# Performance work log

Hardware: AMD Instinct MI355X
Metric: run time of the kernel (lower is better)

The kernel has to match this reference:

```python
import jax, jax.numpy as jnp
import numpy as np

N_NODES = 50000
N_EDGES = 800000
N_GRAPHS = 512
HIDDEN = 256
NODE_FEAT = 9
LAYERS = 4


def setup_inputs() -> dict:
    key = jax.random.key(0)
    ks = jax.random.split(key, 9)
    x = jax.random.normal(ks[0], (N_NODES, NODE_FEAT), dtype=jnp.float32)
    edge_index = jax.random.randint(ks[1], (2, N_EDGES), 0, N_NODES, dtype=jnp.int64)
    batch = jnp.sort(jax.random.randint(ks[2], (N_NODES,), 0, N_GRAPHS, dtype=jnp.int64))
    embed_W = jax.random.normal(ks[3], (NODE_FEAT, HIDDEN), dtype=jnp.float32) * (1.0 / np.sqrt(NODE_FEAT))
    embed_b = jnp.zeros((HIDDEN,), dtype=jnp.float32)
    conv_W = jax.random.normal(ks[4], (LAYERS, HIDDEN, HIDDEN), dtype=jnp.float32) * (1.0 / np.sqrt(HIDDEN))
    conv_b = jnp.zeros((LAYERS, HIDDEN), dtype=jnp.float32)
    out_W = jax.random.normal(ks[5], (HIDDEN, 1), dtype=jnp.float32) * (1.0 / np.sqrt(HIDDEN))
    out_b = jnp.zeros((1,), dtype=jnp.float32)
    return {"x": x, "edge_index": edge_index, "batch": batch,
            "embed_W": embed_W, "embed_b": embed_b,
            "conv_W": conv_W, "conv_b": conv_b,
            "out_W": out_W, "out_b": out_b}


def reference(x, edge_index, batch, embed_W, embed_b, conv_W, conv_b, out_W, out_b):
    n = x.shape[0]
    src, dst = edge_index[0], edge_index[1]
    # GCN symmetric normalization with self-loops: deg includes the self-loop (+1)
    deg = jax.ops.segment_sum(jnp.ones(src.shape[0], x.dtype), dst, num_segments=n) + 1.0
    dinv = jax.lax.rsqrt(deg)                       # [N]
    norm_e = dinv[src] * dinv[dst]                  # [E] edge coefficient
    self_coef = (dinv * dinv)[:, None]              # [N,1] self-loop coefficient

    h = jax.nn.relu(x @ embed_W + embed_b)          # [N,H]
    for l in range(conv_W.shape[0]):
        hw = h @ conv_W[l]                          # [N,H] transform first
        msg = hw[src] * norm_e[:, None]             # [E,H] gather + scale
        agg = jax.ops.segment_sum(msg, dst, num_segments=n)  # scatter-add
        agg = agg + hw * self_coef                  # self-loop contribution
        h = jax.nn.relu(agg + conv_b[l])

    # global mean pool over graph ids
    sums = jax.ops.segment_sum(h, batch, num_segments=N_GRAPHS)           # [G,H]
    cnt = jax.ops.segment_sum(jnp.ones(n, h.dtype), batch, num_segments=N_GRAPHS)
    pooled = sums / jnp.maximum(cnt, 1.0)[:, None]
    return pooled @ out_W + out_b                   # [G,1]
```

## Files before the change

kernel.cpp:

```cpp
#include <hip/hip_runtime.h>

#define N_NODES 50000
#define N_EDGES 800000
#define N_GRAPHS 512
#define HIDDEN 256
#define NODE_FEAT 9
#define LAYERS 4
#define BUCKET 64

typedef float floatx4 __attribute__((ext_vector_type(4)));
typedef short short8 __attribute__((ext_vector_type(8)));

__device__ __forceinline__ float bf2f(unsigned u) {
    unsigned v = u << 16;
    float f;
    __builtin_memcpy(&f, &v, 4);
    return f;
}
__device__ __forceinline__ unsigned short f2bf(float f) {
    unsigned v;
    __builtin_memcpy(&v, &f, 4);
    v += 0x7FFFu + ((v >> 16) & 1u);
    return (unsigned short)(v >> 16);
}

__global__ void fillb_kernel(const int* __restrict__ src, const int* __restrict__ dst,
                             int* __restrict__ cnt, int* __restrict__ col_src, int E) {
    int e = blockIdx.x * blockDim.x + threadIdx.x;
    if (e < E) {
        int d = dst[e];
        int pos = atomicAdd(&cnt[d], 1);
        if (pos < BUCKET) col_src[d * BUCKET + pos] = src[e];
    }
}

__global__ void dinv_kernel(const int* __restrict__ cnt, float* __restrict__ dinv, int N) {
    int i = blockIdx.x * blockDim.x + threadIdx.x;
    if (i < N) dinv[i] = rsqrtf((float)(cnt[i] + 1));
}

__global__ void findstart_kernel(const int* __restrict__ batch, int* __restrict__ gstart) {
    int g = blockIdx.x * blockDim.x + threadIdx.x;
    if (g > N_GRAPHS) return;
    if (g == N_GRAPHS) { gstart[g] = N_NODES; return; }
    int lo = 0, hi = N_NODES;
    while (lo < hi) {
        int mid = (lo + hi) >> 1;
        if (batch[mid] < g) lo = mid + 1; else hi = mid;
    }
    gstart[g] = lo;
}

__global__ __launch_bounds__(256) void packW_kernel(const float* __restrict__ W,
                                                    unsigned short* __restrict__ Wsw) {
    int idx = blockIdx.x * 256 + threadIdx.x;
    int lane = idx & 63;
    int ct   = (idx >> 6) & 15;
    int ks   = (idx >> 10) & 7;
    int l    = idx >> 13;
    int n = ct * 16 + (lane & 15);
    int kbase = ks * 32 + (lane >> 4) * 8;
    const float* Wl = W + (size_t)l * HIDDEN * HIDDEN;
    alignas(16) unsigned short tmp[8];
    #pragma unroll
    for (int j = 0; j < 8; j++)
        tmp[j] = f2bf(Wl[(size_t)(kbase + j) * HIDDEN + n]);
    *(uint4*)&Wsw[(size_t)idx * 8] = *(const uint4*)tmp;
}

__global__ __launch_bounds__(256) void embed_kernel(const float* __restrict__ x,
                                                    const float* __restrict__ W,
                                                    const float* __restrict__ b,
                                                    unsigned short* __restrict__ h) {
    int n = blockIdx.x;
    int c = threadIdx.x;
    float acc = b[c];
    #pragma unroll
    for (int k = 0; k < NODE_FEAT; k++)
        acc += x[n * NODE_FEAT + k] * W[k * HIDDEN + c];
    h[(size_t)n * HIDDEN + c] = f2bf(fmaxf(acc, 0.0f));
}

__global__ __launch_bounds__(256, 2) void gemm_mfma(const unsigned short* __restrict__ hin,
                                                    const unsigned short* __restrict__ Wsw,
                                                    unsigned short* __restrict__ hwout, int N) {
    __shared__ unsigned short As[64][264];
    int t = threadIdx.x;
    int wv = t >> 6, lane = t & 63, quad = lane >> 4, l15 = lane & 15;
    int n0 = blockIdx.x * 64;
    const uint4* h4 = (const uint4*)hin;

    uint4 av[8];
    #pragma unroll
    for (int i = 0; i < 8; i++) {
        int j = t + i * 256;
        int r = j >> 5;
        int c = j & 31;
        int n = n0 + r;
        av[i] = make_uint4(0u, 0u, 0u, 0u);
        if (n < N) av[i] = h4[(size_t)n * 32 + c];
    }
    const short8* Wl = (const short8*)Wsw;
    short8 bq[3][4];
    #pragma unroll
    for (int p = 0; p < 2; p++)
        #pragma unroll
        for (int ci = 0; ci < 4; ci++)
            bq[p][ci] = Wl[(size_t)(p * 16 + wv * 4 + ci) * 64 + lane];
    #pragma unroll
    for (int i = 0; i < 8; i++) {
        int j = t + i * 256;
        int r = j >> 5;
        int c = j & 31;
        *(uint4*)&As[r][c * 8] = av[i];
    }
    __syncthreads();

    floatx4 acc[4][4];
    #pragma unroll
    for (int i = 0; i < 4; i++)
        #pragma unroll
        for (int j = 0; j < 4; j++)
            acc[i][j] = (floatx4){0.f, 0.f, 0.f, 0.f};

    #pragma unroll
    for (int ks = 0; ks < 8; ks++) {
        if (ks < 6) {
            #pragma unroll
            for (int ci = 0; ci < 4; ci++)
                bq[(ks + 2) % 3][ci] = Wl[(size_t)((ks + 2) * 16 + wv * 4 + ci) * 64 + lane];
        }
        short8 a[4];
        #pragma unroll
        for (int rt = 0; rt < 4; rt++)
            a[rt] = *(const short8*)&As[rt * 16 + l15][ks * 32 + quad * 8];
        #pragma unroll
        for (int rt = 0; rt < 4; rt++)
            #pragma unroll
            for (int ci = 0; ci < 4; ci++)
                acc[rt][ci] = __builtin_amdgcn_mfma_f32_16x16x32_bf16(a[rt], bq[ks % 3][ci], acc[rt][ci], 0, 0, 0);
    }

    __syncthreads();
    #pragma unroll
    for (int rt = 0; rt < 4; rt++) {
        #pragma unroll
        for (int ci = 0; ci < 4; ci++) {
            int col = (wv * 4 + ci) * 16 + l15;
            int rowb = rt * 16 + quad * 4;
            #pragma unroll
            for (int reg = 0; reg < 4; reg++)
                As[rowb + reg][col] = f2bf(acc[rt][ci][reg]);
        }
    }
    __syncthreads();
    #pragma unroll
    for (int i = 0; i < 8; i++) {
        int j = t + i * 256;
        int r = j >> 5;
        int c = j & 31;
        int n = n0 + r;
        if (n < N)
            *(uint4*)&hwout[(size_t)n * HIDDEN + c * 8] = *(const uint4*)&As[r][c * 8];
    }
}

__global__ __launch_bounds__(256) void agg_kernel(const unsigned short* __restrict__ hw,
                                                  const int* __restrict__ cnt,
                                                  const int* __restrict__ col_src,
                                                  const float* __restrict__ dinv,
                                                  const float* __restrict__ bias,
                                                  unsigned short* __restrict__ hout) {
    __shared__ uint2 sEdge[4][64];
    int wv = threadIdx.x >> 6, lane = threadIdx.x & 63;
    int n = blockIdx.x * 4 + wv;
    if (n >= N_NODES) return;
    float dn = dinv[n];
    int deg = cnt[n]; if (deg > BUCKET) deg = BUCKET;

    uint2 s2 = ((const uint2*)(hw + (size_t)n * HIDDEN))[lane];
    float4 b4 = *(const float4*)&bias[4 * lane];
    float selfc = dn * dn;
    float a0 = bf2f(s2.x & 0xFFFFu) * selfc + b4.x;
    float a1 = bf2f(s2.x >> 16)     * selfc + b4.y;
    float a2 = bf2f(s2.y & 0xFFFFu) * selfc + b4.z;
    float a3 = bf2f(s2.y >> 16)     * selfc + b4.w;

    if (lane < deg) {
        int s = col_src[n * BUCKET + lane];
        float nr = dinv[s] * dn;
        unsigned nrb;
        __builtin_memcpy(&nrb, &nr, 4);
        sEdge[wv][lane] = make_uint2((unsigned)s, nrb);
    }
    for (int i = 0; i < deg; i++) {
        uint2 p = sEdge[wv][i];
        float nr;
        __builtin_memcpy(&nr, &p.y, 4);
        uint2 u = ((const uint2*)(hw + (size_t)p.x * HIDDEN))[lane];
        a0 += nr * bf2f(u.x & 0xFFFFu);
        a1 += nr * bf2f(u.x >> 16);
        a2 += nr * bf2f(u.y & 0xFFFFu);
        a3 += nr * bf2f(u.y >> 16);
    }
    unsigned p0 = (unsigned)f2bf(fmaxf(a0, 0.0f)) | ((unsigned)f2bf(fmaxf(a1, 0.0f)) << 16);
    unsigned p1 = (unsigned)f2bf(fmaxf(a2, 0.0f)) | ((unsigned)f2bf(fmaxf(a3, 0.0f)) << 16);
    ((uint2*)(hout + (size_t)n * HIDDEN))[lane] = make_uint2(p0, p1);
}

__global__ __launch_bounds__(256) void pool2_kernel(const unsigned short* __restrict__ h,
                                                    const int* __restrict__ gstart,
                                                    const float* __restrict__ outW,
                                                    const float* __restrict__ outb,
                                                    float* __restrict__ out) {
    __shared__ float sred[4];
    int g = blockIdx.x;
    int t = threadIdx.x;
    int s = gstart[g], e = gstart[g + 1];
    int half = t >> 7;
    int tc = t & 127;
    float w0 = outW[2 * tc], w1 = outW[2 * tc + 1];
    float acc = 0.0f;
    for (int n = s + half; n < e; n += 2) {
        unsigned u = *(const unsigned*)&h[(size_t)n * HIDDEN + 2 * tc];
        acc += w0 * bf2f(u & 0xFFFFu) + w1 * bf2f(u >> 16);
    }
    #pragma unroll
    for (int off = 32; off > 0; off >>= 1) acc += __shfl_down(acc, off, 64);
    if ((t & 63) == 0) sred[t >> 6] = acc;
    __syncthreads();
    if (t == 0) {
        float tot = sred[0] + sred[1] + sred[2] + sred[3];
        float cntf = (float)(e - s);
        out[g] = tot / fmaxf(cntf, 1.0f) + outb[0];
    }
}

extern "C" void kernel_launch(void* const* d_in, const int* in_sizes, int n_in,
                              void* d_out, int out_size, void* d_ws, size_t ws_size,
                              hipStream_t stream) {
    const float* x     = (const float*)d_in[0];
    const int*   edge  = (const int*)d_in[1];
    const int*   src   = edge;
    const int*   dst   = edge + N_EDGES;
    const int*   batch = (const int*)d_in[2];
    const float* embW  = (const float*)d_in[3];
    const float* embb  = (const float*)d_in[4];
    const float* convW = (const float*)d_in[5];
    const float* convb = (const float*)d_in[6];
    const float* outW  = (const float*)d_in[7];
    const float* outb  = (const float*)d_in[8];
    float* out = (float*)d_out;

    char* ws = (char*)d_ws;
    size_t off = 0;
    auto take = [&](size_t bytes) { char* p = ws + off; off += (bytes + 255) & ~(size_t)255; return p; };
    int*   cnt     = (int*)  take((size_t)N_NODES * 4);
    int*   col_src = (int*)  take((size_t)N_NODES * BUCKET * 4);
    float* dinv    = (float*)take((size_t)N_NODES * 4);
    int*   gstart  = (int*)  take((size_t)(N_GRAPHS + 1) * 4);
    unsigned short* Wsw = (unsigned short*)take((size_t)LAYERS * 8 * 16 * 64 * 8 * 2);
    unsigned short* h0  = (unsigned short*)take((size_t)N_NODES * HIDDEN * 2);
    unsigned short* h1  = (unsigned short*)take((size_t)N_NODES * HIDDEN * 2);

    hipMemsetAsync(cnt, 0, (size_t)N_NODES * 4, stream);

    fillb_kernel<<<(N_EDGES + 255) / 256, 256, 0, stream>>>(src, dst, cnt, col_src, N_EDGES);
    dinv_kernel<<<(N_NODES + 255) / 256, 256, 0, stream>>>(cnt, dinv, N_NODES);
    findstart_kernel<<<3, 256, 0, stream>>>(batch, gstart);

    packW_kernel<<<128, 256, 0, stream>>>(convW, Wsw);
    embed_kernel<<<N_NODES, 256, 0, stream>>>(x, embW, embb, h0);

    unsigned short* ha = h0;
    unsigned short* hb = h1;
    for (int l = 0; l < LAYERS; l++) {
        gemm_mfma<<<(N_NODES + 63) / 64, 256, 0, stream>>>(ha, Wsw + (size_t)l * 65536, hb, N_NODES);
        agg_kernel<<<(N_NODES + 3) / 4, 256, 0, stream>>>(hb, cnt, col_src, dinv, convb + (size_t)l * HIDDEN, ha);
    }

    pool2_kernel<<<N_GRAPHS, 256, 0, stream>>>(ha, gstart, outW, outb, out);
}
```

Baseline: 459.7 us.

## Split each wavefront across two nodes with 16-byte gathers and unrolled edge loop

```diff
diff --git a/kernel.cpp b/kernel.cpp
--- a/kernel.cpp
+++ b/kernel.cpp
@@ -165,47 +165,87 @@
     }
 }
 
+__device__ __forceinline__ void acc8(float* a, uint4 u, float nr) {
+    a[0] += nr * bf2f(u.x & 0xFFFFu); a[1] += nr * bf2f(u.x >> 16);
+    a[2] += nr * bf2f(u.y & 0xFFFFu); a[3] += nr * bf2f(u.y >> 16);
+    a[4] += nr * bf2f(u.z & 0xFFFFu); a[5] += nr * bf2f(u.z >> 16);
+    a[6] += nr * bf2f(u.w & 0xFFFFu); a[7] += nr * bf2f(u.w >> 16);
+}
+
 __global__ __launch_bounds__(256) void agg_kernel(const unsigned short* __restrict__ hw,
                                                   const int* __restrict__ cnt,
                                                   const int* __restrict__ col_src,
                                                   const float* __restrict__ dinv,
                                                   const float* __restrict__ bias,
                                                   unsigned short* __restrict__ hout) {
-    __shared__ uint2 sEdge[4][64];
+    __shared__ uint2 sEdge[4][2][BUCKET];
     int wv = threadIdx.x >> 6, lane = threadIdx.x & 63;
-    int n = blockIdx.x * 4 + wv;
+    int half = lane >> 5, q = lane & 31;
+    int n = blockIdx.x * 8 + wv * 2 + half;
     if (n >= N_NODES) return;
     float dn = dinv[n];
     int deg = cnt[n]; if (deg > BUCKET) deg = BUCKET;
 
-    uint2 s2 = ((const uint2*)(hw + (size_t)n * HIDDEN))[lane];
-    float4 b4 = *(const float4*)&bias[4 * lane];
+    if (q < deg) {
+        int s = col_src[n * BUCKET + q];
+        float nr = dinv[s] * dn;
+        unsigned nrb; __builtin_memcpy(&nrb, &nr, 4);
+        sEdge[wv][half][q] = make_uint2((unsigned)s, nrb);
+    }
+    if (q + 32 < deg) {
+        int s = col_src[n * BUCKET + q + 32];
+        float nr = dinv[s] * dn;
+        unsigned nrb; __builtin_memcpy(&nrb, &nr, 4);
+        sEdge[wv][half][q + 32] = make_uint2((unsigned)s, nrb);
+    }
+
+    uint4 s4 = ((const uint4*)(hw + (size_t)n * HIDDEN))[q];
     float selfc = dn * dn;
-    float a0 = bf2f(s2.x & 0xFFFFu) * selfc + b4.x;
-    float a1 = bf2f(s2.x >> 16)     * selfc + b4.y;
-    float a2 = bf2f(s2.y & 0xFFFFu) * selfc + b4.z;
-    float a3 = bf2f(s2.y >> 16)     * selfc + b4.w;
-
-    if (lane < deg) {
-        int s = col_src[n * BUCKET + lane];
-        float nr = dinv[s] * dn;
-        unsigned nrb;
-        __builtin_memcpy(&nrb, &nr, 4);
-        sEdge[wv][lane] = make_uint2((unsigned)s, nrb);
-    }
-    for (int i = 0; i < deg; i++) {
-        uint2 p = sEdge[wv][i];
-        float nr;
-        __builtin_memcpy(&nr, &p.y, 4);
-        uint2 u = ((const uint2*)(hw + (size_t)p.x * HIDDEN))[lane];
-        a0 += nr * bf2f(u.x & 0xFFFFu);
-        a1 += nr * bf2f(u.x >> 16);
-        a2 += nr * bf2f(u.y & 0xFFFFu);
-        a3 += nr * bf2f(u.y >> 16);
-    }
-    unsigned p0 = (unsigned)f2bf(fmaxf(a0, 0.0f)) | ((unsigned)f2bf(fmaxf(a1, 0.0f)) << 16);
-    unsigned p1 = (unsigned)f2bf(fmaxf(a2, 0.0f)) | ((unsigned)f2bf(fmaxf(a3, 0.0f)) << 16);
-    ((uint2*)(hout + (size_t)n * HIDDEN))[lane] = make_uint2(p0, p1);
+    float4 b0 = *(const float4*)&bias[8 * q];
+    float4 b1 = *(const float4*)&bias[8 * q + 4];
+    float a[8];
+    a[0] = bf2f(s4.x & 0xFFFFu) * selfc + b0.x;
+    a[1] = bf2f(s4.x >> 16)     * selfc + b0.y;
+    a[2] = bf2f(s4.y & 0xFFFFu) * selfc + b0.z;
+    a[3] = bf2f(s4.y >> 16)     * selfc + b0.w;
+    a[4] = bf2f(s4.z & 0xFFFFu) * selfc + b1.x;
+    a[5] = bf2f(s4.z >> 16)     * selfc + b1.y;
+    a[6] = bf2f(s4.w & 0xFFFFu) * selfc + b1.z;
+    a[7] = bf2f(s4.w >> 16)     * selfc + b1.w;
+
+    const uint4* hw4 = (const uint4*)hw;
+    int i = 0;
+    for (; i + 4 <= deg; i += 4) {
+        uint2 p0 = sEdge[wv][half][i];
+        uint2 p1 = sEdge[wv][half][i + 1];
+        uint2 p2 = sEdge[wv][half][i + 2];
+        uint2 p3 = sEdge[wv][half][i + 3];
+        uint4 u0 = hw4[(size_t)p0.x * 32 + q];
+        uint4 u1 = hw4[(size_t)p1.x * 32 + q];
+        uint4 u2 = hw4[(size_t)p2.x * 32 + q];
+        uint4 u3 = hw4[(size_t)p3.x * 32 + q];
+        float nr0, nr1, nr2, nr3;
+        __builtin_memcpy(&nr0, &p0.y, 4);
+        __builtin_memcpy(&nr1, &p1.y, 4);
+        __builtin_memcpy(&nr2, &p2.y, 4);
+        __builtin_memcpy(&nr3, &p3.y, 4);
+        acc8(a, u0, nr0);
+        acc8(a, u1, nr1);
+        acc8(a, u2, nr2);
+        acc8(a, u3, nr3);
+    }
+    for (; i < deg; i++) {
+        uint2 p = sEdge[wv][half][i];
+        uint4 u = hw4[(size_t)p.x * 32 + q];
+        float nr; __builtin_memcpy(&nr, &p.y, 4);
+        acc8(a, u, nr);
+    }
+
+    unsigned r0 = (unsigned)f2bf(fmaxf(a[0], 0.0f)) | ((unsigned)f2bf(fmaxf(a[1], 0.0f)) << 16);
+    unsigned r1 = (unsigned)f2bf(fmaxf(a[2], 0.0f)) | ((unsigned)f2bf(fmaxf(a[3], 0.0f)) << 16);
+    unsigned r2 = (unsigned)f2bf(fmaxf(a[4], 0.0f)) | ((unsigned)f2bf(fmaxf(a[5], 0.0f)) << 16);
+    unsigned r3 = (unsigned)f2bf(fmaxf(a[6], 0.0f)) | ((unsigned)f2bf(fmaxf(a[7], 0.0f)) << 16);
+    ((uint4*)(hout + (size_t)n * HIDDEN))[q] = make_uint4(r0, r1, r2, r3);
 }
 
 __global__ __launch_bounds__(256) void pool2_kernel(const unsigned short* __restrict__ h,
@@ -276,7 +316,7 @@
     unsigned short* hb = h1;
     for (int l = 0; l < LAYERS; l++) {
         gemm_mfma<<<(N_NODES + 63) / 64, 256, 0, stream>>>(ha, Wsw + (size_t)l * 65536, hb, N_NODES);
-        agg_kernel<<<(N_NODES + 3) / 4, 256, 0, stream>>>(hb, cnt, col_src, dinv, convb + (size_t)l * HIDDEN, ha);
+        agg_kernel<<<(N_NODES + 7) / 8, 256, 0, stream>>>(hb, cnt, col_src, dinv, convb + (size_t)l * HIDDEN, ha);
     }
 
     pool2_kernel<<<N_GRAPHS, 256, 0, stream>>>(ha, gstart, outW, outb, out);
```

New measurement: 459.4 us. No clear change (-0.0%).

## Fuse embedding into first GEMM and fold output projection into last aggregation

Applied to the files above, without the earlier changes.

```diff
diff --git a/kernel.cpp b/kernel.cpp
--- a/kernel.cpp
+++ b/kernel.cpp
@@ -10,6 +10,7 @@
 
 typedef float floatx4 __attribute__((ext_vector_type(4)));
 typedef short short8 __attribute__((ext_vector_type(8)));
+typedef unsigned uint2v __attribute__((ext_vector_type(2)));
 
 __device__ __forceinline__ float bf2f(unsigned u) {
     unsigned v = u << 16;
@@ -68,17 +69,102 @@
     *(uint4*)&Wsw[(size_t)idx * 8] = *(const uint4*)tmp;
 }
 
-__global__ __launch_bounds__(256) void embed_kernel(const float* __restrict__ x,
-                                                    const float* __restrict__ W,
-                                                    const float* __restrict__ b,
-                                                    unsigned short* __restrict__ h) {
-    int n = blockIdx.x;
-    int c = threadIdx.x;
-    float acc = b[c];
-    #pragma unroll
-    for (int k = 0; k < NODE_FEAT; k++)
-        acc += x[n * NODE_FEAT + k] * W[k * HIDDEN + c];
-    h[(size_t)n * HIDDEN + c] = f2bf(fmaxf(acc, 0.0f));
+__global__ __launch_bounds__(256, 2) void embed_gemm(const float* __restrict__ x,
+                                                     const float* __restrict__ embW,
+                                                     const float* __restrict__ embb,
+                                                     const unsigned short* __restrict__ Wsw,
+                                                     unsigned short* __restrict__ hwout, int N) {
+    __shared__ unsigned short As[64][264];
+    int t = threadIdx.x;
+    int wv = t >> 6, lane = t & 63, quad = lane >> 4, l15 = lane & 15;
+    int n0 = blockIdx.x * 64;
+
+    const short8* Wl = (const short8*)Wsw;
+    short8 bq[3][4];
+    #pragma unroll
+    for (int p = 0; p < 2; p++)
+        #pragma unroll
+        for (int ci = 0; ci < 4; ci++)
+            bq[p][ci] = Wl[(size_t)(p * 16 + wv * 4 + ci) * 64 + lane];
+
+    #pragma unroll 2
+    for (int i = 0; i < 8; i++) {
+        int j = t + i * 256;
+        int r = j >> 5;
+        int c8 = j & 31;
+        int n = n0 + r;
+        unsigned o0 = 0, o1 = 0, o2 = 0, o3 = 0;
+        if (n < N) {
+            float xr[NODE_FEAT];
+            #pragma unroll
+            for (int k = 0; k < NODE_FEAT; k++) xr[k] = x[(size_t)n * NODE_FEAT + k];
+            float4 a0 = *(const float4*)&embb[c8 * 8];
+            float4 a1 = *(const float4*)&embb[c8 * 8 + 4];
+            #pragma unroll
+            for (int k = 0; k < NODE_FEAT; k++) {
+                float4 w0 = *(const float4*)&embW[k * HIDDEN + c8 * 8];
+                float4 w1 = *(const float4*)&embW[k * HIDDEN + c8 * 8 + 4];
+                a0.x += xr[k] * w0.x; a0.y += xr[k] * w0.y;
+                a0.z += xr[k] * w0.z; a0.w += xr[k] * w0.w;
+                a1.x += xr[k] * w1.x; a1.y += xr[k] * w1.y;
+                a1.z += xr[k] * w1.z; a1.w += xr[k] * w1.w;
+            }
+            o0 = (unsigned)f2bf(fmaxf(a0.x, 0.f)) | ((unsigned)f2bf(fmaxf(a0.y, 0.f)) << 16);
+            o1 = (unsigned)f2bf(fmaxf(a0.z, 0.f)) | ((unsigned)f2bf(fmaxf(a0.w, 0.f)) << 16);
+            o2 = (unsigned)f2bf(fmaxf(a1.x, 0.f)) | ((unsigned)f2bf(fmaxf(a1.y, 0.f)) << 16);
+            o3 = (unsigned)f2bf(fmaxf(a1.z, 0.f)) | ((unsigned)f2bf(fmaxf(a1.w, 0.f)) << 16);
+        }
+        *(uint4*)&As[r][c8 * 8] = make_uint4(o0, o1, o2, o3);
+    }
+    __syncthreads();
+
+    floatx4 acc[4][4];
+    #pragma unroll
+    for (int i = 0; i < 4; i++)
+        #pragma unroll
+        for (int j = 0; j < 4; j++)
+            acc[i][j] = (floatx4){0.f, 0.f, 0.f, 0.f};
+
+    #pragma unroll
+    for (int ks = 0; ks < 8; ks++) {
+        if (ks < 6) {
+            #pragma unroll
+            for (int ci = 0; ci < 4; ci++)
+                bq[(ks + 2) % 3][ci] = Wl[(size_t)((ks + 2) * 16 + wv * 4 + ci) * 64 + lane];
+        }
+        short8 a[4];
+        #pragma unroll
+        for (int rt = 0; rt < 4; rt++)
+            a[rt] = *(const short8*)&As[rt * 16 + l15][ks * 32 + quad * 8];
+        #pragma unroll
+        for (int rt = 0; rt < 4; rt++)
+            #pragma unroll
+            for (int ci = 0; ci < 4; ci++)
+                acc[rt][ci] = __builtin_amdgcn_mfma_f32_16x16x32_bf16(a[rt], bq[ks % 3][ci], acc[rt][ci], 0, 0, 0);
+    }
+
+    __syncthreads();
+    #pragma unroll
+    for (int rt = 0; rt < 4; rt++) {
+        #pragma unroll
+        for (int ci = 0; ci < 4; ci++) {
+            int col = (wv * 4 + ci) * 16 + l15;
+            int rowb = rt * 16 + quad * 4;
+            #pragma unroll
+            for (int reg = 0; reg < 4; reg++)
+                As[rowb + reg][col] = f2bf(acc[rt][ci][reg]);
+        }
+    }
+    __syncthreads();
+    #pragma unroll
+    for (int i = 0; i < 8; i++) {
+        int j = t + i * 256;
+        int r = j >> 5;
+        int c = j & 31;
+        int n = n0 + r;
+        if (n < N)
+            *(uint4*)&hwout[(size_t)n * HIDDEN + c * 8] = *(const uint4*)&As[r][c * 8];
+    }
 }
 
 __global__ __launch_bounds__(256, 2) void gemm_mfma(const unsigned short* __restrict__ hin,
@@ -205,35 +291,69 @@
     }
     unsigned p0 = (unsigned)f2bf(fmaxf(a0, 0.0f)) | ((unsigned)f2bf(fmaxf(a1, 0.0f)) << 16);
     unsigned p1 = (unsigned)f2bf(fmaxf(a2, 0.0f)) | ((unsigned)f2bf(fmaxf(a3, 0.0f)) << 16);
-    ((uint2*)(hout + (size_t)n * HIDDEN))[lane] = make_uint2(p0, p1);
-}
-
-__global__ __launch_bounds__(256) void pool2_kernel(const unsigned short* __restrict__ h,
-                                                    const int* __restrict__ gstart,
-                                                    const float* __restrict__ outW,
-                                                    const float* __restrict__ outb,
-                                                    float* __restrict__ out) {
-    __shared__ float sred[4];
+    uint2v pv; pv.x = p0; pv.y = p1;
+    __builtin_nontemporal_store(pv, (uint2v*)(hout + (size_t)n * HIDDEN) + lane);
+}
+
+__global__ __launch_bounds__(256) void agg_dot_kernel(const unsigned short* __restrict__ hw,
+                                                      const int* __restrict__ cnt,
+                                                      const int* __restrict__ col_src,
+                                                      const float* __restrict__ dinv,
+                                                      const float* __restrict__ bias,
+                                                      const float* __restrict__ outW,
+                                                      float* __restrict__ dotv) {
+    __shared__ uint2 sEdge[4][64];
+    int wv = threadIdx.x >> 6, lane = threadIdx.x & 63;
+    int n = blockIdx.x * 4 + wv;
+    if (n >= N_NODES) return;
+    float dn = dinv[n];
+    int deg = cnt[n]; if (deg > BUCKET) deg = BUCKET;
+
+    uint2 s2 = ((const uint2*)(hw + (size_t)n * HIDDEN))[lane];
+    float4 b4 = *(const float4*)&bias[4 * lane];
+    float selfc = dn * dn;
+    float a0 = bf2f(s2.x & 0xFFFFu) * selfc + b4.x;
+    float a1 = bf2f(s2.x >> 16)     * selfc + b4.y;
+    float a2 = bf2f(s2.y & 0xFFFFu) * selfc + b4.z;
+    float a3 = bf2f(s2.y >> 16)     * selfc + b4.w;
+
+    if (lane < deg) {
+        int s = col_src[n * BUCKET + lane];
+        float nr = dinv[s] * dn;
+        unsigned nrb;
+        __builtin_memcpy(&nrb, &nr, 4);
+        sEdge[wv][lane] = make_uint2((unsigned)s, nrb);
+    }
+    for (int i = 0; i < deg; i++) {
+        uint2 p = sEdge[wv][i];
+        float nr;
+        __builtin_memcpy(&nr, &p.y, 4);
+        uint2 u = ((const uint2*)(hw + (size_t)p.x * HIDDEN))[lane];
+        a0 += nr * bf2f(u.x & 0xFFFFu);
+        a1 += nr * bf2f(u.x >> 16);
+        a2 += nr * bf2f(u.y & 0xFFFFu);
+        a3 += nr * bf2f(u.y >> 16);
+    }
+    float4 w = *(const float4*)&outW[4 * lane];
+    float dot = fmaxf(a0, 0.0f) * w.x + fmaxf(a1, 0.0f) * w.y
+              + fmaxf(a2, 0.0f) * w.z + fmaxf(a3, 0.0f) * w.w;
+    #pragma unroll
+    for (int off = 32; off > 0; off >>= 1) dot += __shfl_xor(dot, off, 64);
+    if (lane == 0) dotv[n] = dot;
+}
+
+__global__ __launch_bounds__(64) void finalize_kernel(const float* __restrict__ dotv,
+                                                      const int* __restrict__ gstart,
+                                                      const float* __restrict__ outb,
+                                                      float* __restrict__ out) {
     int g = blockIdx.x;
-    int t = threadIdx.x;
+    int lane = threadIdx.x;
     int s = gstart[g], e = gstart[g + 1];
-    int half = t >> 7;
-    int tc = t & 127;
-    float w0 = outW[2 * tc], w1 = outW[2 * tc + 1];
     float acc = 0.0f;
-    for (int n = s + half; n < e; n += 2) {
-        unsigned u = *(const unsigned*)&h[(size_t)n * HIDDEN + 2 * tc];
-        acc += w0 * bf2f(u & 0xFFFFu) + w1 * bf2f(u >> 16);
-    }
-    #pragma unroll
-    for (int off = 32; off > 0; off >>= 1) acc += __shfl_down(acc, off, 64);
-    if ((t & 63) == 0) sred[t >> 6] = acc;
-    __syncthreads();
-    if (t == 0) {
-        float tot = sred[0] + sred[1] + sred[2] + sred[3];
-        float cntf = (float)(e - s);
-        out[g] = tot / fmaxf(cntf, 1.0f) + outb[0];
-    }
+    for (int n = s + lane; n < e; n += 64) acc += dotv[n];
+    #pragma unroll
+    for (int off = 32; off > 0; off >>= 1) acc += __shfl_xor(acc, off, 64);
+    if (lane == 0) out[g] = acc / fmaxf((float)(e - s), 1.0f) + outb[0];
 }
 
 extern "C" void kernel_launch(void* const* d_in, const int* in_sizes, int n_in,
@@ -259,6 +379,7 @@
     int*   col_src = (int*)  take((size_t)N_NODES * BUCKET * 4);
     float* dinv    = (float*)take((size_t)N_NODES * 4);
     int*   gstart  = (int*)  take((size_t)(N_GRAPHS + 1) * 4);
+    float* dotv    = (float*)take((size_t)N_NODES * 4);
     unsigned short* Wsw = (unsigned short*)take((size_t)LAYERS * 8 * 16 * 64 * 8 * 2);
     unsigned short* h0  = (unsigned short*)take((size_t)N_NODES * HIDDEN * 2);
     unsigned short* h1  = (unsigned short*)take((size_t)N_NODES * HIDDEN * 2);
@@ -268,16 +389,19 @@
     fillb_kernel<<<(N_EDGES + 255) / 256, 256, 0, stream>>>(src, dst, cnt, col_src, N_EDGES);
     dinv_kernel<<<(N_NODES + 255) / 256, 256, 0, stream>>>(cnt, dinv, N_NODES);
     findstart_kernel<<<3, 256, 0, stream>>>(batch, gstart);
-
     packW_kernel<<<128, 256, 0, stream>>>(convW, Wsw);
-    embed_kernel<<<N_NODES, 256, 0, stream>>>(x, embW, embb, h0);
-
-    unsigned short* ha = h0;
-    unsigned short* hb = h1;
-    for (int l = 0; l < LAYERS; l++) {
-        gemm_mfma<<<(N_NODES + 63) / 64, 256, 0, stream>>>(ha, Wsw + (size_t)l * 65536, hb, N_NODES);
-        agg_kernel<<<(N_NODES + 3) / 4, 256, 0, stream>>>(hb, cnt, col_src, dinv, convb + (size_t)l * HIDDEN, ha);
-    }
-
-    pool2_kernel<<<N_GRAPHS, 256, 0, stream>>>(ha, gstart, outW, outb, out);
-}
+
+    int nblk = (N_NODES + 63) / 64;
+    int ablk = (N_NODES + 3) / 4;
+
+    embed_gemm<<<nblk, 256, 0, stream>>>(x, embW, embb, Wsw, h1, N_NODES);
+    agg_kernel<<<ablk, 256, 0, stream>>>(h1, cnt, col_src, dinv, convb + 0 * HIDDEN, h0);
+    gemm_mfma<<<nblk, 256, 0, stream>>>(h0, Wsw + (size_t)1 * 65536, h1, N_NODES);
+    agg_kernel<<<ablk, 256, 0, stream>>>(h1, cnt, col_src, dinv, convb + 1 * HIDDEN, h0);
+    gemm_mfma<<<nblk, 256, 0, stream>>>(h0, Wsw + (size_t)2 * 65536, h1, N_NODES);
+    agg_kernel<<<ablk, 256, 0, stream>>>(h1, cnt, col_src, dinv, convb + 2 * HIDDEN, h0);
+    gemm_mfma<<<nblk, 256, 0, stream>>>(h0, Wsw + (size_t)3 * 65536, h1, N_NODES);
+    agg_dot_kernel<<<ablk, 256, 0, stream>>>(h1, cnt, col_src, dinv, convb + 3 * HIDDEN, outW, dotv);
+
+    finalize_kernel<<<N_GRAPHS, 64, 0, stream>>>(dotv, gstart, outb, out);
+}
```

Result: faster. 436.0 us (-5.1%).
